# Performance work log

Measured on AMD Instinct MI355X. Metric: run time of the kernel, lower is better.

## Reference

```python
import jax, jax.numpy as jnp
import numpy as np

# --- module constants (from init_kwargs) ---
R_HRS = 1000000.0   # high-resistance state (ohm)
R_LRS = 1000.0      # low-resistance state (ohm)
PARASITIC_R = 2.0   # wire resistance per crossbar segment (ohm)
BITS = 4            # conductance quantization bits
BATCH, IN_F, OUT_F = 8192, 1024, 1024


def weight_mapping(W, R_hrs, R_lrs):
    # linearly map weights into the [G_hrs, G_lrs] conductance window
    G_hrs, G_lrs = 1.0 / R_hrs, 1.0 / R_lrs
    Wmin, Wmax = W.min(), W.max()
    return (W - Wmin) / (Wmax - Wmin) * (G_lrs - G_hrs) + G_hrs


def quantization(G, R_lrs, R_hrs, bits):
    # snap conductances to 2**bits uniform levels in [G_hrs, G_lrs]
    G_hrs, G_lrs = 1.0 / R_hrs, 1.0 / R_lrs
    step = (G_lrs - G_hrs) / (2 ** bits - 1)
    return jnp.round((G - G_hrs) / step) * step + G_hrs


def ideal_model(G, x, parasitic_r):
    # ideal crossbar: I = V @ G  (no IR drop)
    return x @ G


def jeong_model(G, x, parasitic_r):
    # Jeong-style analytical IR-drop model: each cell (i, j) sees an extra
    # series wire resistance r*((j+1) segments along its word line +
    # (rows - i) segments along its bit line).
    rows, cols = G.shape  # [in, out]
    r_series = parasitic_r * (
        (jnp.arange(cols, dtype=G.dtype) + 1.0)[None, :]
        + (rows - jnp.arange(rows, dtype=G.dtype))[:, None]
    )  # [in, out]
    G_eff = 1.0 / (1.0 / G + r_series)
    return x @ G_eff  # [batch, out]


def output_unmapping(Wt, currents, x, R_hrs, R_lrs):
    # invert the affine conductance mapping: G = a*W + b  =>  x@W = (I - b*sum(x))/a
    G_hrs, G_lrs = 1.0 / R_hrs, 1.0 / R_lrs
    Wmin, Wmax = Wt.min(), Wt.max()
    a = (G_lrs - G_hrs) / (Wmax - Wmin)
    b = G_hrs - a * Wmin
    return (currents - b * x.sum(axis=1, keepdims=True)) / a


def setup_inputs() -> dict:
    key = jax.random.key(0)
    k1, k2, k3 = jax.random.split(key, 3)
    x = jax.random.uniform(k1, (BATCH, IN_F), dtype=jnp.float32)          # read voltages in [0,1)
    weight = jax.random.normal(k2, (OUT_F, IN_F), dtype=jnp.float32) * 0.1
    bias = jax.random.normal(k3, (OUT_F,), dtype=jnp.float32) * 0.01
    return {"x": x, "weight": weight, "bias": bias}


def reference(x, weight, bias):
    Wt = weight.T  # [in, out], matches self.weight.T in the torch module
    conductances = quantization(weight_mapping(Wt, R_HRS, R_LRS), R_LRS, R_HRS, BITS)
    currents = jeong_model(conductances, x, PARASITIC_R)          # non-ideal simulation
    ideal_currents = ideal_model(conductances, x, PARASITIC_R)    # bias-correction pass
    correction = currents.mean(axis=1) / ideal_currents.mean(axis=1)  # [batch]
    output = output_unmapping(Wt, currents, x, R_HRS, R_LRS)      # [batch, out]
    return output + bias[None, :] * correction[:, None]
```

## Files before the change

### kernel.cpp

```cpp
#include <hip/hip_runtime.h>
#include <hip/hip_bf16.h>
#include <cstdint>

#define BATCH 8192
#define IN_F  1024
#define OUT_F 1024
#define G_HRS 1e-6f
#define G_LRS 1e-3f
#define PAR_R 2.0f
#define LEVELS 15.0f

#define WS_PMIN  0
#define WS_PMAX  1024
#define WS_VEFF  4096
#define WS_VID   8192
#define WS_CORR  16384
#define WS_BT    65536
#define WS_ABF   (65536 + 2097152)
#define WS_NEED_FULL  ((size_t)WS_ABF + (size_t)BATCH * IN_F * 2)

__device__ __forceinline__ unsigned short f2bf(float f) {
    union { float f; unsigned int i; } v; v.f = f;
    unsigned int u = v.i;
    unsigned int r = (u + 0x7FFFu + ((u >> 16) & 1u)) >> 16;
    return (unsigned short)r;
}
__device__ __forceinline__ float quant_g(float wv, float wmin, float inv_range) {
    float t = (wv - wmin) * inv_range;
    float step = (G_LRS - G_HRS) / LEVELS;
    return rintf(t * LEVELS) * step + G_HRS;
}

__global__ void kprep(const float* __restrict__ w, float* __restrict__ pmin, float* __restrict__ pmax,
                      float* __restrict__ veff, float* __restrict__ vid) {
    int tid = blockIdx.x * blockDim.x + threadIdx.x;
    float lo = 1e30f, hi = -1e30f;
    const float4* w4 = (const float4*)w;
    const int n4 = (IN_F * OUT_F) / 4;
    for (int i = tid; i < n4; i += 256 * 256) {
        float4 q = w4[i];
        lo = fminf(lo, fminf(fminf(q.x, q.y), fminf(q.z, q.w)));
        hi = fmaxf(hi, fmaxf(fmaxf(q.x, q.y), fmaxf(q.z, q.w)));
    }
#pragma unroll
    for (int m = 1; m < 64; m <<= 1) {
        lo = fminf(lo, __shfl_xor(lo, m, 64));
        hi = fmaxf(hi, __shfl_xor(hi, m, 64));
    }
    __shared__ float slo[4], shi[4];
    int wv = threadIdx.x >> 6, ln = threadIdx.x & 63;
    if (ln == 0) { slo[wv] = lo; shi[wv] = hi; }
    __syncthreads();
    if (threadIdx.x == 0) {
        pmin[blockIdx.x] = fminf(fminf(slo[0], slo[1]), fminf(slo[2], slo[3]));
        pmax[blockIdx.x] = fmaxf(fmaxf(shi[0], shi[1]), fmaxf(shi[2], shi[3]));
    }
    if (blockIdx.x == 0) {
        float4 z = make_float4(0.f, 0.f, 0.f, 0.f);
        ((float4*)veff)[threadIdx.x] = z;
        ((float4*)vid)[threadIdx.x]  = z;
    }
}

__global__ void kbuildvec(const float* __restrict__ w, const float* __restrict__ pmin,
                          const float* __restrict__ pmax, unsigned short* __restrict__ bt,
                          float* __restrict__ veff, float* __restrict__ vid) {
    float lo = pmin[threadIdx.x], hi = pmax[threadIdx.x];
#pragma unroll
    for (int m = 1; m < 64; m <<= 1) {
        lo = fminf(lo, __shfl_xor(lo, m, 64));
        hi = fmaxf(hi, __shfl_xor(hi, m, 64));
    }
    __shared__ float slo[4], shi[4];
    int wv = threadIdx.x >> 6, ln = threadIdx.x & 63;
    if (ln == 0) { slo[wv] = lo; shi[wv] = hi; }
    __syncthreads();
    float wmin = fminf(fminf(slo[0], slo[1]), fminf(slo[2], slo[3]));
    float wmax = fmaxf(fmaxf(shi[0], shi[1]), fmaxf(shi[2], shi[3]));

    float inv_range = 1.0f / (wmax - wmin);
    float acoef = (G_LRS - G_HRS) * inv_range;
    float bcoef = G_HRS - acoef * wmin;
    float inva = 1.0f / acoef;

    int k0 = threadIdx.x * 4;
    float se[4] = {0.f, 0.f, 0.f, 0.f}, si[4] = {0.f, 0.f, 0.f, 0.f};
#pragma unroll
    for (int rr = 0; rr < 4; rr++) {
        int n = blockIdx.x * 4 + rr;
        float4 q = *(const float4*)&w[(size_t)n * IN_F + k0];
        float wvv[4] = { q.x, q.y, q.z, q.w };
        unsigned short o[4];
#pragma unroll
        for (int j = 0; j < 4; j++) {
            int k = k0 + j;
            float g = quant_g(wvv[j], wmin, inv_range);
            float r = PAR_R * ((float)(n + 1) + (float)(IN_F - k));
            float ge = 1.0f / (1.0f / g + r);
            o[j] = f2bf((ge - bcoef) * inva);
            se[j] += ge;
            si[j] += g;
        }
        uint2 ov;
        ov.x = (unsigned int)o[0] | ((unsigned int)o[1] << 16);
        ov.y = (unsigned int)o[2] | ((unsigned int)o[3] << 16);
        *(uint2*)&bt[(size_t)n * IN_F + k0] = ov;
    }
#pragma unroll
    for (int j = 0; j < 4; j++) {
        atomicAdd(&veff[k0 + j], se[j]);
        atomicAdd(&vid[k0 + j], si[j]);
    }
}

__global__ void kcorr(const float* __restrict__ x, const float* __restrict__ veff,
                      const float* __restrict__ vid, float* __restrict__ corr,
                      unsigned short* __restrict__ abf) {
    int row = blockIdx.x * 4 + (threadIdx.x >> 6);
    int lane = threadIdx.x & 63;
    int k0 = lane * 16;
    const float* xr = x + (size_t)row * IN_F + k0;
    float se = 0.f, si = 0.f;
#pragma unroll
    for (int p = 0; p < 4; p++) {
        float4 q  = *(const float4*)(xr + p * 4);
        float4 ve = *(const float4*)(veff + k0 + p * 4);
        float4 vi = *(const float4*)(vid  + k0 + p * 4);
        se += q.x * ve.x + q.y * ve.y + q.z * ve.z + q.w * ve.w;
        si += q.x * vi.x + q.y * vi.y + q.z * vi.z + q.w * vi.w;
        if (abf) {
            uint2 ov;
            ov.x = (unsigned int)f2bf(q.x) | ((unsigned int)f2bf(q.y) << 16);
            ov.y = (unsigned int)f2bf(q.z) | ((unsigned int)f2bf(q.w) << 16);
            *(uint2*)&abf[(size_t)row * IN_F + k0 + p * 4] = ov;
        }
    }
#pragma unroll
    for (int m = 1; m < 64; m <<= 1) {
        se += __shfl_xor(se, m, 64);
        si += __shfl_xor(si, m, 64);
    }
    if (lane == 0) corr[row] = se / si;
}

typedef __attribute__((ext_vector_type(8))) short bf16x8;
typedef __attribute__((ext_vector_type(4))) float f32x4;

#define GLD_LDS16(g, l) \
    __builtin_amdgcn_global_load_lds((const __attribute__((address_space(1))) void*)(g), \
                                     (__attribute__((address_space(3))) void*)(l), 16, 0, 0)

template <bool CONVA>
__global__ __launch_bounds__(256) void kgemm(
    const float* __restrict__ Af32,
    const unsigned short* __restrict__ Abf,
    const unsigned short* __restrict__ Bt,
    const float* __restrict__ bias,
    const float* __restrict__ corr,
    float* __restrict__ out)
{
    __shared__ unsigned short As0[128 * 32];
    __shared__ unsigned short As1[128 * 32];
    __shared__ unsigned short Bs0[128 * 32];
    __shared__ unsigned short Bs1[128 * 32];
    const int tid = threadIdx.x;
    const int f = blockIdx.x;
    const int bm = ((f & 7) * 8 + ((f >> 3) & 7)) * 128;
    const int bn = (f >> 6) * 128;
    const int wave = tid >> 6, lane = tid & 63;
    const int wmL = (wave >> 1) * 64;
    const int wnL = (wave & 1) * 64;
    const int fr = lane & 15;
    const int fk = (lane >> 4) * 8;
    const int quad = lane >> 4;

    f32x4 acc[4][4] = {};

    const int c0 = tid, c1 = tid + 256;
    const unsigned short* gB0 = Bt + (size_t)(bn + (c0 >> 2)) * IN_F + ((c0 & 3) << 3);
    const unsigned short* gB1 = Bt + (size_t)(bn + (c1 >> 2)) * IN_F + ((c1 & 3) << 3);
    const unsigned short* gA0 = nullptr; const unsigned short* gA1 = nullptr;
    const float* fA0 = nullptr; const float* fA1 = nullptr;
    if (CONVA) {
        fA0 = Af32 + (size_t)(bm + (c0 >> 2)) * IN_F + ((c0 & 3) << 3);
        fA1 = Af32 + (size_t)(bm + (c1 >> 2)) * IN_F + ((c1 & 3) << 3);
    } else {
        gA0 = Abf + (size_t)(bm + (c0 >> 2)) * IN_F + ((c0 & 3) << 3);
        gA1 = Abf + (size_t)(bm + (c1 >> 2)) * IN_F + ((c1 & 3) << 3);
    }

    for (int kb = 0; kb < IN_F; kb += 64) {
        if (CONVA) {
            float4 p[8];
            p[0] = *(const float4*)(fA0 + kb);      p[1] = *(const float4*)(fA0 + kb + 4);
            p[2] = *(const float4*)(fA1 + kb);      p[3] = *(const float4*)(fA1 + kb + 4);
            p[4] = *(const float4*)(fA0 + kb + 32); p[5] = *(const float4*)(fA0 + kb + 36);
            p[6] = *(const float4*)(fA1 + kb + 32); p[7] = *(const float4*)(fA1 + kb + 36);
            uint4 u[4];
#pragma unroll
            for (int j = 0; j < 4; j++) {
                u[j] = make_uint4(
                    (unsigned int)f2bf(p[2*j].x) | ((unsigned int)f2bf(p[2*j].y) << 16),
                    (unsigned int)f2bf(p[2*j].z) | ((unsigned int)f2bf(p[2*j].w) << 16),
                    (unsigned int)f2bf(p[2*j+1].x) | ((unsigned int)f2bf(p[2*j+1].y) << 16),
                    (unsigned int)f2bf(p[2*j+1].z) | ((unsigned int)f2bf(p[2*j+1].w) << 16));
            }
            __syncthreads();
            *(uint4*)&As0[c0 * 8] = u[0];
            *(uint4*)&As0[c1 * 8] = u[1];
            *(uint4*)&As1[c0 * 8] = u[2];
            *(uint4*)&As1[c1 * 8] = u[3];
            GLD_LDS16(gB0 + kb, &Bs0[c0 * 8]);
            GLD_LDS16(gB1 + kb, &Bs0[c1 * 8]);
            GLD_LDS16(gB0 + kb + 32, &Bs1[c0 * 8]);
            GLD_LDS16(gB1 + kb + 32, &Bs1[c1 * 8]);
        } else {
            __syncthreads();
            GLD_LDS16(gA0 + kb,      &As0[c0 * 8]);
            GLD_LDS16(gA1 + kb,      &As0[c1 * 8]);
            GLD_LDS16(gB0 + kb,      &Bs0[c0 * 8]);
            GLD_LDS16(gB1 + kb,      &Bs0[c1 * 8]);
            GLD_LDS16(gA0 + kb + 32, &As1[c0 * 8]);
            GLD_LDS16(gA1 + kb + 32, &As1[c1 * 8]);
            GLD_LDS16(gB0 + kb + 32, &Bs1[c0 * 8]);
            GLD_LDS16(gB1 + kb + 32, &Bs1[c1 * 8]);
        }
        __syncthreads();

        bf16x8 af[4], bfv[4];
#pragma unroll
        for (int mt = 0; mt < 4; mt++)
            af[mt] = *(const bf16x8*)&As0[(wmL + mt * 16 + fr) * 32 + fk];
#pragma unroll
        for (int nt = 0; nt < 4; nt++)
            bfv[nt] = *(const bf16x8*)&Bs0[(wnL + nt * 16 + fr) * 32 + fk];
#pragma unroll
        for (int mt = 0; mt < 4; mt++)
#pragma unroll
            for (int nt = 0; nt < 4; nt++)
                acc[mt][nt] = __builtin_amdgcn_mfma_f32_16x16x32_bf16(af[mt], bfv[nt], acc[mt][nt], 0, 0, 0);
#pragma unroll
        for (int mt = 0; mt < 4; mt++)
            af[mt] = *(const bf16x8*)&As1[(wmL + mt * 16 + fr) * 32 + fk];
#pragma unroll
        for (int nt = 0; nt < 4; nt++)
            bfv[nt] = *(const bf16x8*)&Bs1[(wnL + nt * 16 + fr) * 32 + fk];
#pragma unroll
        for (int mt = 0; mt < 4; mt++)
#pragma unroll
            for (int nt = 0; nt < 4; nt++)
                acc[mt][nt] = __builtin_amdgcn_mfma_f32_16x16x32_bf16(af[mt], bfv[nt], acc[mt][nt], 0, 0, 0);
    }

#pragma unroll
    for (int nt = 0; nt < 4; nt++) {
        int gc = bn + wnL + nt * 16 + fr;
        float bv = bias[gc];
#pragma unroll
        for (int mt = 0; mt < 4; mt++) {
#pragma unroll
            for (int r = 0; r < 4; r++) {
                int gr = bm + wmL + mt * 16 + quad * 4 + r;
                out[(size_t)gr * OUT_F + gc] = acc[mt][nt][r] + bv * corr[gr];
            }
        }
    }
}

extern "C" void kernel_launch(void* const* d_in, const int* in_sizes, int n_in,
                              void* d_out, int out_size, void* d_ws, size_t ws_size,
                              hipStream_t stream) {
    const float* x    = (const float*)d_in[0];
    const float* w    = (const float*)d_in[1];
    const float* bias = (const float*)d_in[2];
    float* out = (float*)d_out;

    char* ws = (char*)d_ws;
    float* pmin        = (float*)(ws + WS_PMIN);
    float* pmax        = (float*)(ws + WS_PMAX);
    float* veff        = (float*)(ws + WS_VEFF);
    float* vid         = (float*)(ws + WS_VID);
    float* corr        = (float*)(ws + WS_CORR);
    unsigned short* bt = (unsigned short*)(ws + WS_BT);
    unsigned short* abf = (unsigned short*)(ws + WS_ABF);

    bool full = ws_size >= WS_NEED_FULL;

    kprep<<<256, 256, 0, stream>>>(w, pmin, pmax, veff, vid);
    kbuildvec<<<OUT_F / 4, 256, 0, stream>>>(w, pmin, pmax, bt, veff, vid);
    kcorr<<<BATCH / 4, 256, 0, stream>>>(x, veff, vid, corr, full ? abf : nullptr);
    if (full)
        kgemm<false><<<512, 256, 0, stream>>>(x, abf, bt, bias, corr, out);
    else
        kgemm<true><<<512, 256, 0, stream>>>(x, nullptr, bt, bias, corr, out);
}
```

Measured before the change: 147.3 us.

## Rewrite bf16 GEMM with double-buffered swizzled LDS and interleaved prefetch

Replaces the templated GEMM with a dedicated kernel that uses a 64-wide K tile, two LDS buffers with XOR swizzling to avoid bank conflicts, and issues next-tile global-to-LDS loads interleaved with MFMA groups, using explicit waitcnt, barriers and setprio. This aims to hide global load latency and cut the per-iteration syncthreads stalls of the single-stage loop. The weight-building kernel also processes 16 rows per block instead of 4. Hand-placed waitcnt counts make correctness fragile if the load ordering assumptions are wrong.

```diff
diff --git a/kernel.cpp b/kernel.cpp
--- a/kernel.cpp
+++ b/kernel.cpp
@@ -86,8 +86,8 @@
     int k0 = threadIdx.x * 4;
     float se[4] = {0.f, 0.f, 0.f, 0.f}, si[4] = {0.f, 0.f, 0.f, 0.f};
 #pragma unroll
-    for (int rr = 0; rr < 4; rr++) {
-        int n = blockIdx.x * 4 + rr;
+    for (int rr = 0; rr < 16; rr++) {
+        int n = blockIdx.x * 16 + rr;
         float4 q = *(const float4*)&w[(size_t)n * IN_F + k0];
         float wvv[4] = { q.x, q.y, q.z, q.w };
         unsigned short o[4];
@@ -150,10 +150,201 @@
     __builtin_amdgcn_global_load_lds((const __attribute__((address_space(1))) void*)(g), \
                                      (__attribute__((address_space(3))) void*)(l), 16, 0, 0)
 
-template <bool CONVA>
-__global__ __launch_bounds__(256) void kgemm(
+#define LGKM0 do { asm volatile("s_waitcnt lgkmcnt(0)" ::: "memory"); \
+                   __builtin_amdgcn_sched_barrier(0); } while (0)
+#define VMCNT(n) asm volatile("s_waitcnt vmcnt(" #n ")" ::: "memory")
+#define SBAR     asm volatile("s_barrier" ::: "memory")
+
+#define MFMA_ROW(MT, A) \
+    acc[MT][0] = __builtin_amdgcn_mfma_f32_16x16x32_bf16(A, b0, acc[MT][0], 0, 0, 0); \
+    acc[MT][1] = __builtin_amdgcn_mfma_f32_16x16x32_bf16(A, b1, acc[MT][1], 0, 0, 0); \
+    acc[MT][2] = __builtin_amdgcn_mfma_f32_16x16x32_bf16(A, b2, acc[MT][2], 0, 0, 0); \
+    acc[MT][3] = __builtin_amdgcn_mfma_f32_16x16x32_bf16(A, b3, acc[MT][3], 0, 0, 0);
+
+__global__ __launch_bounds__(256) void kgemm2(
+    const unsigned short* __restrict__ Abf,
+    const unsigned short* __restrict__ Bt,
+    const float* __restrict__ bias,
+    const float* __restrict__ corr,
+    float* __restrict__ out)
+{
+    __shared__ unsigned short As[2 * 128 * 64];
+    __shared__ unsigned short Bs[2 * 128 * 64];
+    const int tid = threadIdx.x;
+    const int f = blockIdx.x;
+    const int bm = ((f & 7) * 8 + ((f >> 3) & 7)) * 128;
+    const int bn = (f >> 6) * 128;
+    const int wave = tid >> 6, lane = tid & 63;
+    const int wmL = (wave >> 1) * 64;
+    const int wnL = (wave & 1) * 64;
+    const int fr = lane & 15;
+    const int quad = lane >> 4;
+
+    const int sw   = (fr & 7) * 16;
+    const int aRd0 = (wmL + fr) * 128 + ((quad * 16) ^ sw);
+    const int aRd1 = (wmL + fr) * 128 + (((64 + quad * 16)) ^ sw);
+    const int bRd0 = (wnL + fr) * 128 + ((quad * 16) ^ sw);
+    const int bRd1 = (wnL + fr) * 128 + (((64 + quad * 16)) ^ sw);
+
+    const int arow  = tid >> 3;
+    const int acolb = ((tid & 7) * 16) ^ ((arow & 7) * 16);
+    const unsigned short* gA = Abf + (size_t)(bm + arow) * IN_F + (acolb >> 1);
+    const unsigned short* gB = Bt  + (size_t)(bn + arow) * IN_F + (acolb >> 1);
+
+    f32x4 acc[4][4] = {};
+
+    {
+        unsigned short* lA = As + tid * 8;
+        unsigned short* lB = Bs + tid * 8;
+        GLD_LDS16(gB,              lB);
+        GLD_LDS16(gB + 32 * IN_F,  lB + 2048);
+        GLD_LDS16(gB + 64 * IN_F,  lB + 4096);
+        GLD_LDS16(gB + 96 * IN_F,  lB + 6144);
+        GLD_LDS16(gA,              lA);
+        GLD_LDS16(gA + 32 * IN_F,  lA + 2048);
+        GLD_LDS16(gA + 64 * IN_F,  lA + 4096);
+        GLD_LDS16(gA + 96 * IN_F,  lA + 6144);
+        VMCNT(0);
+        SBAR;
+    }
+
+#pragma unroll 1
+    for (int t = 0; t < 15; ++t) {
+        const int rb = (t & 1) << 13;
+        const int wb = rb ^ 8192;
+        const int kbn = t * 64 + 64;
+        const char* Ar = (const char*)(As + rb);
+        const char* Br = (const char*)(Bs + rb);
+        unsigned short* Aw = As + wb + tid * 8;
+        unsigned short* Bw = Bs + wb + tid * 8;
+        bf16x8 b0, b1, b2, b3, a0, a1;
+
+        b0 = *(const bf16x8*)(Br + bRd0);
+        b1 = *(const bf16x8*)(Br + bRd0 + 2048);
+        b2 = *(const bf16x8*)(Br + bRd0 + 4096);
+        b3 = *(const bf16x8*)(Br + bRd0 + 6144);
+        a0 = *(const bf16x8*)(Ar + aRd0);
+        a1 = *(const bf16x8*)(Ar + aRd0 + 2048);
+        GLD_LDS16(gB + kbn,             Bw);
+        GLD_LDS16(gB + 32 * IN_F + kbn, Bw + 2048);
+        LGKM0;
+        __builtin_amdgcn_s_setprio(1);
+        MFMA_ROW(0, a0)
+        MFMA_ROW(1, a1)
+        __builtin_amdgcn_s_setprio(0);
+        __builtin_amdgcn_sched_barrier(0);
+        VMCNT(2);
+        SBAR;
+
+        a0 = *(const bf16x8*)(Ar + aRd0 + 4096);
+        a1 = *(const bf16x8*)(Ar + aRd0 + 6144);
+        GLD_LDS16(gB + 64 * IN_F + kbn, Bw + 4096);
+        GLD_LDS16(gB + 96 * IN_F + kbn, Bw + 6144);
+        LGKM0;
+        __builtin_amdgcn_s_setprio(1);
+        MFMA_ROW(2, a0)
+        MFMA_ROW(3, a1)
+        __builtin_amdgcn_s_setprio(0);
+        __builtin_amdgcn_sched_barrier(0);
+
+        b0 = *(const bf16x8*)(Br + bRd1);
+        b1 = *(const bf16x8*)(Br + bRd1 + 2048);
+        b2 = *(const bf16x8*)(Br + bRd1 + 4096);
+        b3 = *(const bf16x8*)(Br + bRd1 + 6144);
+        a0 = *(const bf16x8*)(Ar + aRd1);
+        a1 = *(const bf16x8*)(Ar + aRd1 + 2048);
+        GLD_LDS16(gA + kbn,             Aw);
+        GLD_LDS16(gA + 64 * IN_F + kbn, Aw + 4096);
+        LGKM0;
+        __builtin_amdgcn_s_setprio(1);
+        MFMA_ROW(0, a0)
+        MFMA_ROW(1, a1)
+        __builtin_amdgcn_s_setprio(0);
+        __builtin_amdgcn_sched_barrier(0);
+
+        a0 = *(const bf16x8*)(Ar + aRd1 + 4096);
+        a1 = *(const bf16x8*)(Ar + aRd1 + 6144);
+        GLD_LDS16(gA + 32 * IN_F + kbn, Aw + 2048);
+        GLD_LDS16(gA + 96 * IN_F + kbn, Aw + 6144);
+        LGKM0;
+        __builtin_amdgcn_s_setprio(1);
+        MFMA_ROW(2, a0)
+        MFMA_ROW(3, a1)
+        __builtin_amdgcn_s_setprio(0);
+        __builtin_amdgcn_sched_barrier(0);
+        VMCNT(2);
+        SBAR;
+    }
+
+    {
+        const char* Ar = (const char*)(As + 8192);
+        const char* Br = (const char*)(Bs + 8192);
+        bf16x8 b0, b1, b2, b3, a0, a1;
+
+        b0 = *(const bf16x8*)(Br + bRd0);
+        b1 = *(const bf16x8*)(Br + bRd0 + 2048);
+        b2 = *(const bf16x8*)(Br + bRd0 + 4096);
+        b3 = *(const bf16x8*)(Br + bRd0 + 6144);
+        a0 = *(const bf16x8*)(Ar + aRd0);
+        a1 = *(const bf16x8*)(Ar + aRd0 + 2048);
+        LGKM0;
+        __builtin_amdgcn_s_setprio(1);
+        MFMA_ROW(0, a0)
+        MFMA_ROW(1, a1)
+        __builtin_amdgcn_s_setprio(0);
+        __builtin_amdgcn_sched_barrier(0);
+        VMCNT(0);
+        SBAR;
+
+        a0 = *(const bf16x8*)(Ar + aRd0 + 4096);
+        a1 = *(const bf16x8*)(Ar + aRd0 + 6144);
+        LGKM0;
+        __builtin_amdgcn_s_setprio(1);
+        MFMA_ROW(2, a0)
+        MFMA_ROW(3, a1)
+        __builtin_amdgcn_s_setprio(0);
+        __builtin_amdgcn_sched_barrier(0);
+
+        b0 = *(const bf16x8*)(Br + bRd1);
+        b1 = *(const bf16x8*)(Br + bRd1 + 2048);
+        b2 = *(const bf16x8*)(Br + bRd1 + 4096);
+        b3 = *(const bf16x8*)(Br + bRd1 + 6144);
+        a0 = *(const bf16x8*)(Ar + aRd1);
+        a1 = *(const bf16x8*)(Ar + aRd1 + 2048);
+        LGKM0;
+        __builtin_amdgcn_s_setprio(1);
+        MFMA_ROW(0, a0)
+        MFMA_ROW(1, a1)
+        __builtin_amdgcn_s_setprio(0);
+        __builtin_amdgcn_sched_barrier(0);
+
+        a0 = *(const bf16x8*)(Ar + aRd1 + 4096);
+        a1 = *(const bf16x8*)(Ar + aRd1 + 6144);
+        LGKM0;
+        __builtin_amdgcn_s_setprio(1);
+        MFMA_ROW(2, a0)
+        MFMA_ROW(3, a1)
+        __builtin_amdgcn_s_setprio(0);
+        __builtin_amdgcn_sched_barrier(0);
+    }
+
+#pragma unroll
+    for (int nt = 0; nt < 4; nt++) {
+        int gc = bn + wnL + nt * 16 + fr;
+        float bv = bias[gc];
+#pragma unroll
+        for (int mt = 0; mt < 4; mt++) {
+#pragma unroll
+            for (int r = 0; r < 4; r++) {
+                int gr = bm + wmL + mt * 16 + quad * 4 + r;
+                out[(size_t)gr * OUT_F + gc] = acc[mt][nt][r] + bv * corr[gr];
+            }
+        }
+    }
+}
+
+__global__ __launch_bounds__(256) void kgemm_conva(
     const float* __restrict__ Af32,
-    const unsigned short* __restrict__ Abf,
     const unsigned short* __restrict__ Bt,
     const float* __restrict__ bias,
     const float* __restrict__ corr,
@@ -179,52 +370,33 @@
     const int c0 = tid, c1 = tid + 256;
     const unsigned short* gB0 = Bt + (size_t)(bn + (c0 >> 2)) * IN_F + ((c0 & 3) << 3);
     const unsigned short* gB1 = Bt + (size_t)(bn + (c1 >> 2)) * IN_F + ((c1 & 3) << 3);
-    const unsigned short* gA0 = nullptr; const unsigned short* gA1 = nullptr;
-    const float* fA0 = nullptr; const float* fA1 = nullptr;
-    if (CONVA) {
-        fA0 = Af32 + (size_t)(bm + (c0 >> 2)) * IN_F + ((c0 & 3) << 3);
-        fA1 = Af32 + (size_t)(bm + (c1 >> 2)) * IN_F + ((c1 & 3) << 3);
-    } else {
-        gA0 = Abf + (size_t)(bm + (c0 >> 2)) * IN_F + ((c0 & 3) << 3);
-        gA1 = Abf + (size_t)(bm + (c1 >> 2)) * IN_F + ((c1 & 3) << 3);
-    }
+    const float* fA0 = Af32 + (size_t)(bm + (c0 >> 2)) * IN_F + ((c0 & 3) << 3);
+    const float* fA1 = Af32 + (size_t)(bm + (c1 >> 2)) * IN_F + ((c1 & 3) << 3);
 
     for (int kb = 0; kb < IN_F; kb += 64) {
-        if (CONVA) {
-            float4 p[8];
-            p[0] = *(const float4*)(fA0 + kb);      p[1] = *(const float4*)(fA0 + kb + 4);
-            p[2] = *(const float4*)(fA1 + kb);      p[3] = *(const float4*)(fA1 + kb + 4);
-            p[4] = *(const float4*)(fA0 + kb + 32); p[5] = *(const float4*)(fA0 + kb + 36);
-            p[6] = *(const float4*)(fA1 + kb + 32); p[7] = *(const float4*)(fA1 + kb + 36);
-            uint4 u[4];
-#pragma unroll
-            for (int j = 0; j < 4; j++) {
-                u[j] = make_uint4(
-                    (unsigned int)f2bf(p[2*j].x) | ((unsigned int)f2bf(p[2*j].y) << 16),
-                    (unsigned int)f2bf(p[2*j].z) | ((unsigned int)f2bf(p[2*j].w) << 16),
-                    (unsigned int)f2bf(p[2*j+1].x) | ((unsigned int)f2bf(p[2*j+1].y) << 16),
-                    (unsigned int)f2bf(p[2*j+1].z) | ((unsigned int)f2bf(p[2*j+1].w) << 16));
-            }
-            __syncthreads();
-            *(uint4*)&As0[c0 * 8] = u[0];
-            *(uint4*)&As0[c1 * 8] = u[1];
-            *(uint4*)&As1[c0 * 8] = u[2];
-            *(uint4*)&As1[c1 * 8] = u[3];
-            GLD_LDS16(gB0 + kb, &Bs0[c0 * 8]);
-            GLD_LDS16(gB1 + kb, &Bs0[c1 * 8]);
-            GLD_LDS16(gB0 + kb + 32, &Bs1[c0 * 8]);
-            GLD_LDS16(gB1 + kb + 32, &Bs1[c1 * 8]);
-        } else {
-            __syncthreads();
-            GLD_LDS16(gA0 + kb,      &As0[c0 * 8]);
-            GLD_LDS16(gA1 + kb,      &As0[c1 * 8]);
-            GLD_LDS16(gB0 + kb,      &Bs0[c0 * 8]);
-            GLD_LDS16(gB1 + kb,      &Bs0[c1 * 8]);
-            GLD_LDS16(gA0 + kb + 32, &As1[c0 * 8]);
-            GLD_LDS16(gA1 + kb + 32, &As1[c1 * 8]);
-            GLD_LDS16(gB0 + kb + 32, &Bs1[c0 * 8]);
-            GLD_LDS16(gB1 + kb + 32, &Bs1[c1 * 8]);
+        float4 p[8];
+        p[0] = *(const float4*)(fA0 + kb);      p[1] = *(const float4*)(fA0 + kb + 4);
+        p[2] = *(const float4*)(fA1 + kb);      p[3] = *(const float4*)(fA1 + kb + 4);
+        p[4] = *(const float4*)(fA0 + kb + 32); p[5] = *(const float4*)(fA0 + kb + 36);
+        p[6] = *(const float4*)(fA1 + kb + 32); p[7] = *(const float4*)(fA1 + kb + 36);
+        uint4 u[4];
+#pragma unroll
+        for (int j = 0; j < 4; j++) {
+            u[j] = make_uint4(
+                (unsigned int)f2bf(p[2*j].x) | ((unsigned int)f2bf(p[2*j].y) << 16),
+                (unsigned int)f2bf(p[2*j].z) | ((unsigned int)f2bf(p[2*j].w) << 16),
+                (unsigned int)f2bf(p[2*j+1].x) | ((unsigned int)f2bf(p[2*j+1].y) << 16),
+                (unsigned int)f2bf(p[2*j+1].z) | ((unsigned int)f2bf(p[2*j+1].w) << 16));
         }
+        __syncthreads();
+        *(uint4*)&As0[c0 * 8] = u[0];
+        *(uint4*)&As0[c1 * 8] = u[1];
+        *(uint4*)&As1[c0 * 8] = u[2];
+        *(uint4*)&As1[c1 * 8] = u[3];
+        GLD_LDS16(gB0 + kb, &Bs0[c0 * 8]);
+        GLD_LDS16(gB1 + kb, &Bs0[c1 * 8]);
+        GLD_LDS16(gB0 + kb + 32, &Bs1[c0 * 8]);
+        GLD_LDS16(gB1 + kb + 32, &Bs1[c1 * 8]);
         __syncthreads();
 
         bf16x8 af[4], bfv[4];
@@ -287,10 +459,10 @@
     bool full = ws_size >= WS_NEED_FULL;
 
     kprep<<<256, 256, 0, stream>>>(w, pmin, pmax, veff, vid);
-    kbuildvec<<<OUT_F / 4, 256, 0, stream>>>(w, pmin, pmax, bt, veff, vid);
+    kbuildvec<<<OUT_F / 16, 256, 0, stream>>>(w, pmin, pmax, bt, veff, vid);
     kcorr<<<BATCH / 4, 256, 0, stream>>>(x, veff, vid, corr, full ? abf : nullptr);
     if (full)
-        kgemm<false><<<512, 256, 0, stream>>>(x, abf, bt, bias, corr, out);
+        kgemm2<<<512, 256, 0, stream>>>(abf, bt, bias, corr, out);
     else
-        kgemm<true><<<512, 256, 0, stream>>>(x, nullptr, bt, bias, corr, out);
-}
+        kgemm_conva<<<512, 256, 0, stream>>>(x, bt, bias, corr, out);
+}
```

Result: faster. 133.6 us (-9.3%).
